# Performance work log

Measured on AMD Instinct MI355X. Metric: run time of the kernel, lower is better.

## Reference

```python
import jax, jax.numpy as jnp
import numpy as np

B, H, W, K, PAD = 1024, 28, 28, 3, 1


def conv3x3(x, w, b):
    out = jax.lax.conv_general_dilated(x, w, (1, 1), ((PAD, PAD), (PAD, PAD)),
                                       dimension_numbers=('NCHW', 'OIHW', 'NCHW'))
    return out + b[None, :, None, None]


def deform_conv2d(x, offset, w, b):
    # torchvision deform_conv2d semantics, stride=1, pad=1, dilation=1, groups=1
    Bn, Cin, Hh, Ww = x.shape
    Cout = w.shape[0]
    KK = K * K
    off = offset.reshape(Bn, KK, 2, Hh, Ww)
    dy, dx = off[:, :, 0], off[:, :, 1]                      # [B,KK,H,W]
    ky, kx = jnp.meshgrid(jnp.arange(K, dtype=x.dtype), jnp.arange(K, dtype=x.dtype), indexing='ij')
    py = dy + (jnp.arange(Hh, dtype=x.dtype) - PAD)[None, None, :, None] + ky.reshape(KK)[None, :, None, None]
    px = dx + (jnp.arange(Ww, dtype=x.dtype) - PAD)[None, None, None, :] + kx.reshape(KK)[None, :, None, None]
    y0 = jnp.floor(py); x0 = jnp.floor(px)
    wy1 = py - y0; wy0 = 1.0 - wy1
    wx1 = px - x0; wx0 = 1.0 - wx1
    xf = x.reshape(Bn, Cin, Hh * Ww)

    def gather(yi, xi):
        valid = (yi >= 0) & (yi < Hh) & (xi >= 0) & (xi < Ww)
        yc = jnp.clip(yi, 0, Hh - 1).astype(jnp.int32)
        xc = jnp.clip(xi, 0, Ww - 1).astype(jnp.int32)
        idx = (yc * Ww + xc).reshape(Bn, -1)                 # [B, KK*H*W]
        g = jnp.take_along_axis(xf, jnp.broadcast_to(idx[:, None, :], (Bn, Cin, idx.shape[1])), axis=2)
        return g.reshape(Bn, Cin, KK, Hh, Ww) * valid.astype(x.dtype)[:, None]

    sampled = (gather(y0, x0) * (wy0 * wx0)[:, None]
               + gather(y0, x0 + 1) * (wy0 * wx1)[:, None]
               + gather(y0 + 1, x0) * (wy1 * wx0)[:, None]
               + gather(y0 + 1, x0 + 1) * (wy1 * wx1)[:, None])  # [B,Cin,KK,H,W]
    out = jnp.einsum('bkhw,ok->bohw', sampled.reshape(Bn, Cin * KK, Hh, Ww),
                     w.reshape(Cout, Cin * KK))
    return out + b[None, :, None, None]


def adaptive_avg_pool_14(x):
    Bn, C, Hh, Ww = x.shape
    f = Hh // 14
    return x.reshape(Bn, C, 14, f, 14, f).mean(axis=(3, 5))


def setup_inputs() -> dict:
    key = jax.random.key(0)
    ks = jax.random.split(key, 14)
    d = {}
    d['x'] = jax.random.normal(ks[0], (B, 1, H, W), dtype=jnp.float32)
    # offset conv 1: Conv2d(1, 18, 3, pad=1)
    d['ow1'] = jax.random.normal(ks[1], (18, 1, 3, 3), dtype=jnp.float32) * 0.1
    d['ob1'] = jnp.zeros((18,), jnp.float32)
    d['w1'] = jax.random.normal(ks[2], (32, 1, 3, 3), dtype=jnp.float32) * 0.01
    d['b1'] = jnp.zeros((32,), jnp.float32)
    # offset conv 2: Conv2d(32, 18, 3, pad=1)
    d['ow2'] = jax.random.normal(ks[3], (18, 32, 3, 3), dtype=jnp.float32) * 0.05
    d['ob2'] = jnp.zeros((18,), jnp.float32)
    d['w2'] = jax.random.normal(ks[4], (64, 32, 3, 3), dtype=jnp.float32) * 0.01
    d['b2'] = jnp.zeros((64,), jnp.float32)
    d['fw1'] = jax.random.normal(ks[5], (128, 64 * 14 * 14), dtype=jnp.float32) * 0.01
    d['fb1'] = jnp.zeros((128,), jnp.float32)
    d['fw2'] = jax.random.normal(ks[6], (10, 128), dtype=jnp.float32) * 0.05
    d['fb2'] = jnp.zeros((10,), jnp.float32)
    return d


def reference(x, ow1, ob1, w1, b1, ow2, ob2, w2, b2, fw1, fb1, fw2, fb2):
    # block1 + relu + pool 28->14
    h = deform_conv2d(x, conv3x3(x, ow1, ob1), w1, b1)
    h = adaptive_avg_pool_14(jax.nn.relu(h))
    # block2 + relu + pool 14->14 (identity)
    h = deform_conv2d(h, conv3x3(h, ow2, ob2), w2, b2)
    h = adaptive_avg_pool_14(jax.nn.relu(h))
    h = h.reshape(h.shape[0], -1)
    # classifier (ExcitationDropout is identity in eval mode)
    h = jax.nn.relu(h @ fw1.T + fb1)
    return h @ fw2.T + fb2
```

## Files before the change

### kernel.cpp

```cpp
#include <hip/hip_runtime.h>

#define NB 1024
#define TOTAL1 (NB*196)

#define WS_H1   0
#define WS_H2   6422528
#define WS_PART 19267584
#define WS_W1T  23461888
#define WS_OW1T 23462176
#define WS_W2T  23462338
#define WS_OW2T 23480770

__global__ __launch_bounds__(256) void prep(const float* __restrict__ w1,
                                            const float* __restrict__ ow1,
                                            const float* __restrict__ w2,
                                            const float* __restrict__ ow2,
                                            float* __restrict__ ws) {
  int i = blockIdx.x * 256 + threadIdx.x;
  if (i < 288)   { int co = i / 9,  kk = i % 9;   ws[WS_W1T  + kk * 32 + co] = w1[i]; }
  if (i < 162)   { int c  = i / 9,  j  = i % 9;   ws[WS_OW1T + j  * 18 + c ] = ow1[i]; }
  if (i < 18432) { int co = i / 288, k = i % 288; ws[WS_W2T  + k  * 64 + co] = w2[i]; }
  if (i < 5184)  { int c  = i / 288, k = i % 288; ws[WS_OW2T + k  * 18 + c ] = ow2[i]; }
}

__global__ __launch_bounds__(256, 2) void stage1(const float* __restrict__ x,
                                                 const float* __restrict__ ob1,
                                                 const float* __restrict__ b1,
                                                 const float* __restrict__ ws,
                                                 float* __restrict__ h1) {
  __shared__ float ximg[3 * 784];
  const float* __restrict__ w1t  = ws + WS_W1T;
  const float* __restrict__ ow1t = ws + WS_OW1T;
  int tid = threadIdx.x;
  int g0 = blockIdx.x * 256;
  int bfirst = g0 / 196;
  for (int idx = tid; idx < 3 * 784; idx += 256) {
    int img = idx / 784;
    int b = bfirst + img;
    ximg[idx] = (b < NB) ? x[b * 784 + (idx - img * 784)] : 0.f;
  }
  __syncthreads();
  int g = g0 + tid;
  if (g >= TOTAL1) return;
  int b = g / 196, p = g - b * 196;
  const float* im = ximg + (b - bfirst) * 784;
  int oy = p / 14, ox = p - (p / 14) * 14;

  float pooled[32];
#pragma unroll
  for (int co = 0; co < 32; ++co) pooled[co] = 0.f;

  for (int sub = 0; sub < 4; ++sub) {
    int y  = 2 * oy + (sub >> 1);
    int ix = 2 * ox + (sub & 1);
    float patch[9];
#pragma unroll
    for (int j = 0; j < 9; ++j) {
      int yy = y + j / 3 - 1, xc = ix + j % 3 - 1;
      bool ok = (yy >= 0) & (yy < 28) & (xc >= 0) & (xc < 28);
      patch[j] = ok ? im[yy * 28 + xc] : 0.f;
    }
    float off[18];
#pragma unroll
    for (int c = 0; c < 18; ++c) off[c] = ob1[c];
#pragma unroll
    for (int j = 0; j < 9; ++j) {
      float v = patch[j];
#pragma unroll
      for (int c = 0; c < 18; ++c) off[c] = fmaf(v, ow1t[j * 18 + c], off[c]);
    }
    float a[32];
#pragma unroll
    for (int co = 0; co < 32; ++co) a[co] = b1[co];
#pragma unroll
    for (int kk = 0; kk < 9; ++kk) {
      float py = (float)(y - 1 + kk / 3) + off[2 * kk];
      float px = (float)(ix - 1 + kk % 3) + off[2 * kk + 1];
      float y0f = floorf(py), x0f = floorf(px);
      float wy1 = py - y0f, wx1 = px - x0f;
      float wy0 = 1.f - wy1, wx0 = 1.f - wx1;
      int y0 = (int)y0f, x0 = (int)x0f;
      int y1 = y0 + 1, x1 = x0 + 1;
      bool vy0 = (y0 >= 0) & (y0 < 28), vy1 = (y1 >= 0) & (y1 < 28);
      bool vx0 = (x0 >= 0) & (x0 < 28), vx1 = (x1 >= 0) & (x1 < 28);
      float W00 = (vy0 & vx0) ? wy0 * wx0 : 0.f;
      float W01 = (vy0 & vx1) ? wy0 * wx1 : 0.f;
      float W10 = (vy1 & vx0) ? wy1 * wx0 : 0.f;
      float W11 = (vy1 & vx1) ? wy1 * wx1 : 0.f;
      int yc0 = min(max(y0, 0), 27), yc1 = min(max(y1, 0), 27);
      int xc0 = min(max(x0, 0), 27), xc1 = min(max(x1, 0), 27);
      float s = im[yc0 * 28 + xc0] * W00 + im[yc0 * 28 + xc1] * W01 +
                im[yc1 * 28 + xc0] * W10 + im[yc1 * 28 + xc1] * W11;
#pragma unroll
      for (int co = 0; co < 32; ++co) a[co] = fmaf(s, w1t[kk * 32 + co], a[co]);
    }
#pragma unroll
    for (int co = 0; co < 32; ++co) pooled[co] += fmaxf(a[co], 0.f);
  }
#pragma unroll
  for (int co = 0; co < 32; ++co) h1[b * 6272 + co * 196 + p] = pooled[co] * 0.25f;
}

__global__ __launch_bounds__(256, 4) void stage2(const float* __restrict__ h1,
                                                 const float* __restrict__ ob2,
                                                 const float* __restrict__ b2,
                                                 const float* __restrict__ ws,
                                                 float* __restrict__ h2) {
  __shared__ float imgT[196 * 32];
  __shared__ float Sbuf2[2 * 1608];
  const float* __restrict__ w2t  = ws + WS_W2T;
  const float* __restrict__ ow2t = ws + WS_OW2T;
  int tid = threadIdx.x;
  int b = blockIdx.x;

  for (int e = tid; e < 6272; e += 256) {
    int ci = e / 196, p = e - ci * 196;
    imgT[p * 32 + ((ci + 4 * p) & 31)] = h1[b * 6272 + e];
  }

  int pp = tid;
  int spy = pp / 14, spx = pp - (pp / 14) * 14;
  bool samp = (pp < 196);

  int cog = tid & 15, pg = tid >> 4;
  int co0 = cog * 4, p0 = pg * 16;
  bool gact = (pg < 13);
  float acc[4][16];
  {
    float4 bb = *(const float4*)(b2 + co0);
    float bj[4] = {bb.x, bb.y, bb.z, bb.w};
#pragma unroll
    for (int jj = 0; jj < 4; ++jj)
#pragma unroll
      for (int i = 0; i < 16; ++i) acc[jj][i] = bj[jj];
  }

  __syncthreads();

  float off[18];
#pragma unroll
  for (int c = 0; c < 18; ++c) off[c] = ob2[c];
  if (samp) {
    for (int j = 0; j < 9; ++j) {
      int yy = spy + j / 3 - 1, xx = spx + j % 3 - 1;
      bool ok = (yy >= 0) & (yy < 14) & (xx >= 0) & (xx < 14);
      int nidx = ok ? (yy * 14 + xx) : 0;
      const float* src = imgT + nidx * 32;
      int rot = (4 * nidx) & 31;
      for (int cq = 0; cq < 8; ++cq) {
        float4 v;
        if (ok) v = *(const float4*)(src + ((cq * 4 + rot) & 31));
        else    v = make_float4(0.f, 0.f, 0.f, 0.f);
        const float* wo0 = ow2t + ((cq * 4 + 0) * 9 + j) * 18;
        const float* wo1 = ow2t + ((cq * 4 + 1) * 9 + j) * 18;
        const float* wo2 = ow2t + ((cq * 4 + 2) * 9 + j) * 18;
        const float* wo3 = ow2t + ((cq * 4 + 3) * 9 + j) * 18;
#pragma unroll
        for (int c = 0; c < 18; ++c) {
          off[c] = fmaf(v.x, wo0[c], off[c]);
          off[c] = fmaf(v.y, wo1[c], off[c]);
          off[c] = fmaf(v.z, wo2[c], off[c]);
          off[c] = fmaf(v.w, wo3[c], off[c]);
        }
      }
    }
  }

  float W00 = 0.f, W01 = 0.f, W10 = 0.f, W11 = 0.f;
  int s00o = 0, s01o = 0, s10o = 0, s11o = 0;
  int r00 = 0, r01 = 0, r10 = 0, r11 = 0;

  auto coeff = [&](int kkv) {
    float dy = off[0], dx = off[1];
#pragma unroll
    for (int t = 1; t < 9; ++t) if (kkv == t) { dy = off[2 * t]; dx = off[2 * t + 1]; }
    float pyv = (float)(spy - 1 + kkv / 3) + dy;
    float pxv = (float)(spx - 1 + kkv % 3) + dx;
    float y0f = floorf(pyv), x0f = floorf(pxv);
    float wy1 = pyv - y0f, wx1 = pxv - x0f;
    float wy0 = 1.f - wy1, wx0 = 1.f - wx1;
    int y0 = (int)y0f, x0 = (int)x0f;
    int y1 = y0 + 1, x1 = x0 + 1;
    bool vy0 = (y0 >= 0) & (y0 < 14), vy1 = (y1 >= 0) & (y1 < 14);
    bool vx0 = (x0 >= 0) & (x0 < 14), vx1 = (x1 >= 0) & (x1 < 14);
    W00 = (vy0 & vx0) ? wy0 * wx0 : 0.f;
    W01 = (vy0 & vx1) ? wy0 * wx1 : 0.f;
    W10 = (vy1 & vx0) ? wy1 * wx0 : 0.f;
    W11 = (vy1 & vx1) ? wy1 * wx1 : 0.f;
    int yc0 = min(max(y0, 0), 13), yc1 = min(max(y1, 0), 13);
    int xc0 = min(max(x0, 0), 13), xc1 = min(max(x1, 0), 13);
    int i00 = yc0 * 14 + xc0, i01 = yc0 * 14 + xc1;
    int i10 = yc1 * 14 + xc0, i11 = yc1 * 14 + xc1;
    s00o = i00 * 32; r00 = (4 * i00) & 31;
    s01o = i01 * 32; r01 = (4 * i01) & 31;
    s10o = i10 * 32; r10 = (4 * i10) & 31;
    s11o = i11 * 32; r11 = (4 * i11) & 31;
  };

  auto sample = [&](int qn, int bufn) {
    float* dst = Sbuf2 + bufn * 1608 + pp;
#pragma unroll
    for (int cg = 0; cg < 2; ++cg) {
      int gq = qn * 2 + cg;
      float4 a0 = *(const float4*)(imgT + s00o + ((gq * 4 + r00) & 31));
      float4 a1 = *(const float4*)(imgT + s01o + ((gq * 4 + r01) & 31));
      float4 a2 = *(const float4*)(imgT + s10o + ((gq * 4 + r10) & 31));
      float4 a3 = *(const float4*)(imgT + s11o + ((gq * 4 + r11) & 31));
      dst[(cg * 4 + 0) * 200] = fmaf(W00, a0.x, fmaf(W01, a1.x, fmaf(W10, a2.x, W11 * a3.x)));
      dst[(cg * 4 + 1) * 200] = fmaf(W00, a0.y, fmaf(W01, a1.y, fmaf(W10, a2.y, W11 * a3.y)));
      dst[(cg * 4 + 2) * 200] = fmaf(W00, a0.z, fmaf(W01, a1.z, fmaf(W10, a2.z, W11 * a3.z)));
      dst[(cg * 4 + 3) * 200] = fmaf(W00, a0.w, fmaf(W01, a1.w, fmaf(W10, a2.w, W11 * a3.w)));
    }
  };

  if (samp) { coeff(0); sample(0, 0); }
  __syncthreads();

  for (int kk = 0; kk < 9; ++kk) {
#pragma unroll
    for (int q = 0; q < 4; ++q) {
      if (samp && !((kk == 8) & (q == 3))) {
        if (q == 3) coeff(kk + 1);
        sample((q + 1) & 3, (q + 1) & 1);
      }
      if (gact) {
        const float* sb = Sbuf2 + (q & 1) * 1608 + p0;
        const float* wb = w2t + kk * 64 + co0;
#pragma unroll 2
        for (int l = 0; l < 8; ++l) {
          int ci = q * 8 + l;
          float4 w = *(const float4*)(wb + ci * 576);
          const float* srow = sb + l * 200;
          float4 s0 = *(const float4*)(srow);
          float4 s1 = *(const float4*)(srow + 4);
          float4 s2 = *(const float4*)(srow + 8);
          float4 s3 = *(const float4*)(srow + 12);
          float sv[16] = {s0.x, s0.y, s0.z, s0.w, s1.x, s1.y, s1.z, s1.w,
                          s2.x, s2.y, s2.z, s2.w, s3.x, s3.y, s3.z, s3.w};
          float wj[4] = {w.x, w.y, w.z, w.w};
#pragma unroll
          for (int jj = 0; jj < 4; ++jj)
#pragma unroll
            for (int i = 0; i < 16; ++i)
              acc[jj][i] = fmaf(wj[jj], sv[i], acc[jj][i]);
        }
      }
      __syncthreads();
    }
  }

  if (gact) {
    float* __restrict__ orow = h2 + b * 12544 + co0 * 196 + p0;
#pragma unroll
    for (int jj = 0; jj < 4; ++jj) {
#pragma unroll
      for (int t = 0; t < 4; ++t) {
        if (p0 + 4 * t < 196) {
          float4 v;
          v.x = fmaxf(acc[jj][4 * t + 0], 0.f);
          v.y = fmaxf(acc[jj][4 * t + 1], 0.f);
          v.z = fmaxf(acc[jj][4 * t + 2], 0.f);
          v.w = fmaxf(acc[jj][4 * t + 3], 0.f);
          *(float4*)(orow + jj * 196 + 4 * t) = v;
        }
      }
    }
  }
}

__global__ __launch_bounds__(256, 2) void fc1(const float* __restrict__ h2,
                                              const float* __restrict__ fw1,
                                              float* __restrict__ part) {
  __shared__ float a_s[56 * 72];
  __shared__ float b_s[56 * 132];
  int tid = threadIdx.x;
  int rb = (blockIdx.x & 15) * 64;
  int ks = blockIdx.x >> 4;
  int kbase = ks * 392;
  int c0 = (tid & 31) * 4;
  int r0 = (tid >> 5) * 8;

  float acc[8][4];
#pragma unroll
  for (int i = 0; i < 8; ++i)
#pragma unroll
    for (int j = 0; j < 4; ++j) acc[i][j] = 0.f;

  for (int ch = 0; ch < 7; ++ch) {
    int kb = kbase + ch * 56;
    __syncthreads();
#pragma unroll
    for (int t = 0; t < 14; ++t) {
      int idx = t * 256 + tid;
      int r = idx / 56, k = idx - r * 56;
      a_s[k * 72 + r] = h2[(rb + r) * 12544 + kb + k];
    }
#pragma unroll
    for (int t = 0; t < 28; ++t) {
      int idx = t * 256 + tid;
      int c = idx / 56, k = idx - c * 56;
      b_s[k * 132 + c] = fw1[c * 12544 + kb + k];
    }
    __syncthreads();
    for (int k = 0; k < 56; ++k) {
      float4 bv = *(const float4*)&b_s[k * 132 + c0];
      float4 av0 = *(const float4*)&a_s[k * 72 + r0];
      float4 av1 = *(const float4*)&a_s[k * 72 + r0 + 4];
      float av[8] = {av0.x, av0.y, av0.z, av0.w, av1.x, av1.y, av1.z, av1.w};
      float bj[4] = {bv.x, bv.y, bv.z, bv.w};
#pragma unroll
      for (int i = 0; i < 8; ++i)
#pragma unroll
        for (int j = 0; j < 4; ++j) acc[i][j] = fmaf(av[i], bj[j], acc[i][j]);
    }
  }
#pragma unroll
  for (int i = 0; i < 8; ++i) {
    int r = rb + r0 + i;
#pragma unroll
    for (int j = 0; j < 4; ++j)
      part[(ks * 1024 + r) * 128 + c0 + j] = acc[i][j];
  }
}

__global__ __launch_bounds__(128) void fcfinal(const float* __restrict__ part,
                                               const float* __restrict__ fb1,
                                               const float* __restrict__ fw2,
                                               const float* __restrict__ fb2,
                                               float* __restrict__ out) {
  __shared__ float tbuf[128];
  int b = blockIdx.x, c = threadIdx.x;
  float s = fb1[c];
  for (int ks = 0; ks < 32; ++ks) s += part[(ks * 1024 + b) * 128 + c];
  tbuf[c] = fmaxf(s, 0.f);
  __syncthreads();
  if (c < 10) {
    float v = fb2[c];
#pragma unroll
    for (int k = 0; k < 128; ++k) v = fmaf(tbuf[k], fw2[c * 128 + k], v);
    out[b * 10 + c] = v;
  }
}

extern "C" void kernel_launch(void* const* d_in, const int* in_sizes, int n_in,
                              void* d_out, int out_size, void* d_ws, size_t ws_size,
                              hipStream_t stream) {
  const float* x   = (const float*)d_in[0];
  const float* ow1 = (const float*)d_in[1];
  const float* ob1 = (const float*)d_in[2];
  const float* w1  = (const float*)d_in[3];
  const float* b1  = (const float*)d_in[4];
  const float* ow2 = (const float*)d_in[5];
  const float* ob2 = (const float*)d_in[6];
  const float* w2  = (const float*)d_in[7];
  const float* b2  = (const float*)d_in[8];
  const float* fw1 = (const float*)d_in[9];
  const float* fb1 = (const float*)d_in[10];
  const float* fw2 = (const float*)d_in[11];
  const float* fb2 = (const float*)d_in[12];
  float* ws  = (float*)d_ws;
  float* out = (float*)d_out;

  prep<<<72, 256, 0, stream>>>(w1, ow1, w2, ow2, ws);
  stage1<<<784, 256, 0, stream>>>(x, ob1, b1, ws, ws + WS_H1);
  stage2<<<NB, 256, 0, stream>>>(ws + WS_H1, ob2, b2, ws, ws + WS_H2);
  fc1<<<512, 256, 0, stream>>>(ws + WS_H2, fw1, ws + WS_PART);
  fcfinal<<<1024, 128, 0, stream>>>(ws + WS_PART, fb1, fw2, fb2, out);
}
```

Before: 443.1 us.

## Split stage2 offset convolution into a separate kernel writing offsets to workspace

Moves the second offset 3x3 conv (32->18 channels) out of stage2 into a new offconv kernel that processes two images per 448-thread block and writes 18 offset maps to the workspace. Stage2 then loads only the dy/dx pair for the next kernel tap from global memory, which frees the 18 offset registers and removes the idle-thread imbalance where only 196 of 256 threads did the offset conv. The cost is an extra kernel launch, a second read of h1, and a global round trip for the offsets. The offsets reuse the WS_PART region, which is safe only because fc1 overwrites it later.

```diff
diff --git a/kernel.cpp b/kernel.cpp
--- a/kernel.cpp
+++ b/kernel.cpp
@@ -6,6 +6,7 @@
 #define WS_H1   0
 #define WS_H2   6422528
 #define WS_PART 19267584
+#define WS_OFF2 WS_PART
 #define WS_W1T  23461888
 #define WS_OW1T 23462176
 #define WS_W2T  23462338
@@ -101,15 +102,72 @@
   for (int co = 0; co < 32; ++co) h1[b * 6272 + co * 196 + p] = pooled[co] * 0.25f;
 }
 
+__global__ __launch_bounds__(448, 4) void offconv(const float* __restrict__ h1,
+                                                  const float* __restrict__ ob2,
+                                                  const float* __restrict__ ws,
+                                                  float* __restrict__ off2) {
+  __shared__ float imgT[2 * 6272];
+  const float* __restrict__ ow2t = ws + WS_OW2T;
+  int tid = threadIdx.x;
+  int bb = blockIdx.x;
+
+  for (int e = tid; e < 12544; e += 448) {
+    int img = e / 6272, rem = e - img * 6272;
+    int ci = rem / 196, p = rem - ci * 196;
+    imgT[img * 6272 + p * 32 + ((ci + 4 * p) & 31)] = h1[bb * 12544 + e];
+  }
+  __syncthreads();
+
+  int img  = tid / 224;
+  int slot = tid - img * 224;
+  int py  = slot >> 4;
+  int pxc = slot & 15;
+  int pxx = min(pxc, 13);
+  int p   = py * 14 + pxx;
+  const float* im = imgT + img * 6272;
+
+  float off[18];
+#pragma unroll
+  for (int c = 0; c < 18; ++c) off[c] = ob2[c];
+  for (int j = 0; j < 9; ++j) {
+    int yy = py + j / 3 - 1, xx = pxx + j % 3 - 1;
+    bool ok = (yy >= 0) & (yy < 14) & (xx >= 0) & (xx < 14);
+    int nidx = ok ? (yy * 14 + xx) : 0;
+    const float* src = im + nidx * 32;
+    int rot = (4 * nidx) & 31;
+    for (int cq = 0; cq < 8; ++cq) {
+      float4 v;
+      if (ok) v = *(const float4*)(src + ((cq * 4 + rot) & 31));
+      else    v = make_float4(0.f, 0.f, 0.f, 0.f);
+      const float* w0 = ow2t + ((cq * 4 + 0) * 9 + j) * 18;
+      const float* w1 = ow2t + ((cq * 4 + 1) * 9 + j) * 18;
+      const float* w2 = ow2t + ((cq * 4 + 2) * 9 + j) * 18;
+      const float* w3 = ow2t + ((cq * 4 + 3) * 9 + j) * 18;
+#pragma unroll
+      for (int c = 0; c < 18; ++c) {
+        off[c] = fmaf(v.x, w0[c], off[c]);
+        off[c] = fmaf(v.y, w1[c], off[c]);
+        off[c] = fmaf(v.z, w2[c], off[c]);
+        off[c] = fmaf(v.w, w3[c], off[c]);
+      }
+    }
+  }
+
+  if (pxc < 14) {
+    float* dst = off2 + (2 * bb + img) * 3528 + p;
+#pragma unroll
+    for (int c = 0; c < 18; ++c) dst[c * 196] = off[c];
+  }
+}
+
 __global__ __launch_bounds__(256, 4) void stage2(const float* __restrict__ h1,
-                                                 const float* __restrict__ ob2,
+                                                 const float* __restrict__ off2,
                                                  const float* __restrict__ b2,
                                                  const float* __restrict__ ws,
                                                  float* __restrict__ h2) {
   __shared__ float imgT[196 * 32];
   __shared__ float Sbuf2[2 * 1608];
-  const float* __restrict__ w2t  = ws + WS_W2T;
-  const float* __restrict__ ow2t = ws + WS_OW2T;
+  const float* __restrict__ w2t = ws + WS_W2T;
   int tid = threadIdx.x;
   int b = blockIdx.x;
 
@@ -121,6 +179,7 @@
   int pp = tid;
   int spy = pp / 14, spx = pp - (pp / 14) * 14;
   bool samp = (pp < 196);
+  const float* off_b = off2 + b * 3528;
 
   int cog = tid & 15, pg = tid >> 4;
   int co0 = cog * 4, p0 = pg * 16;
@@ -135,47 +194,14 @@
       for (int i = 0; i < 16; ++i) acc[jj][i] = bj[jj];
   }
 
-  __syncthreads();
-
-  float off[18];
-#pragma unroll
-  for (int c = 0; c < 18; ++c) off[c] = ob2[c];
-  if (samp) {
-    for (int j = 0; j < 9; ++j) {
-      int yy = spy + j / 3 - 1, xx = spx + j % 3 - 1;
-      bool ok = (yy >= 0) & (yy < 14) & (xx >= 0) & (xx < 14);
-      int nidx = ok ? (yy * 14 + xx) : 0;
-      const float* src = imgT + nidx * 32;
-      int rot = (4 * nidx) & 31;
-      for (int cq = 0; cq < 8; ++cq) {
-        float4 v;
-        if (ok) v = *(const float4*)(src + ((cq * 4 + rot) & 31));
-        else    v = make_float4(0.f, 0.f, 0.f, 0.f);
-        const float* wo0 = ow2t + ((cq * 4 + 0) * 9 + j) * 18;
-        const float* wo1 = ow2t + ((cq * 4 + 1) * 9 + j) * 18;
-        const float* wo2 = ow2t + ((cq * 4 + 2) * 9 + j) * 18;
-        const float* wo3 = ow2t + ((cq * 4 + 3) * 9 + j) * 18;
-#pragma unroll
-        for (int c = 0; c < 18; ++c) {
-          off[c] = fmaf(v.x, wo0[c], off[c]);
-          off[c] = fmaf(v.y, wo1[c], off[c]);
-          off[c] = fmaf(v.z, wo2[c], off[c]);
-          off[c] = fmaf(v.w, wo3[c], off[c]);
-        }
-      }
-    }
-  }
-
   float W00 = 0.f, W01 = 0.f, W10 = 0.f, W11 = 0.f;
   int s00o = 0, s01o = 0, s10o = 0, s11o = 0;
   int r00 = 0, r01 = 0, r10 = 0, r11 = 0;
+  float dyn = 0.f, dxn = 0.f;
 
   auto coeff = [&](int kkv) {
-    float dy = off[0], dx = off[1];
-#pragma unroll
-    for (int t = 1; t < 9; ++t) if (kkv == t) { dy = off[2 * t]; dx = off[2 * t + 1]; }
-    float pyv = (float)(spy - 1 + kkv / 3) + dy;
-    float pxv = (float)(spx - 1 + kkv % 3) + dx;
+    float pyv = (float)(spy - 1 + kkv / 3) + dyn;
+    float pxv = (float)(spx - 1 + kkv % 3) + dxn;
     float y0f = floorf(pyv), x0f = floorf(pxv);
     float wy1 = pyv - y0f, wx1 = pxv - x0f;
     float wy0 = 1.f - wy1, wx0 = 1.f - wx1;
@@ -213,6 +239,8 @@
     }
   };
 
+  if (samp) { dyn = off_b[pp]; dxn = off_b[196 + pp]; }
+  __syncthreads();
   if (samp) { coeff(0); sample(0, 0); }
   __syncthreads();
 
@@ -220,6 +248,10 @@
 #pragma unroll
     for (int q = 0; q < 4; ++q) {
       if (samp && !((kk == 8) & (q == 3))) {
+        if (q == 1 && kk < 8) {
+          dyn = off_b[(2 * kk + 2) * 196 + pp];
+          dxn = off_b[(2 * kk + 3) * 196 + pp];
+        }
         if (q == 3) coeff(kk + 1);
         sample((q + 1) & 3, (q + 1) & 1);
       }
@@ -363,7 +395,8 @@
 
   prep<<<72, 256, 0, stream>>>(w1, ow1, w2, ow2, ws);
   stage1<<<784, 256, 0, stream>>>(x, ob1, b1, ws, ws + WS_H1);
-  stage2<<<NB, 256, 0, stream>>>(ws + WS_H1, ob2, b2, ws, ws + WS_H2);
+  offconv<<<512, 448, 0, stream>>>(ws + WS_H1, ob2, ws, ws + WS_OFF2);
+  stage2<<<NB, 256, 0, stream>>>(ws + WS_H1, ws + WS_OFF2, b2, ws, ws + WS_H2);
   fc1<<<512, 256, 0, stream>>>(ws + WS_H2, fw1, ws + WS_PART);
   fcfinal<<<1024, 128, 0, stream>>>(ws + WS_PART, fb1, fw2, fb2, out);
 }
```

Result: no change. 448.4 us (+1.2%).

## Compute stage2 offset conv as a cooperative shared-memory GEMM and retile main GEMM to 8x8

Applied to the files above, without the earlier changes.

The offset convolution in stage2 no longer has each sampling thread accumulate all 18 offset channels serially from global weights. Instead, all threads run it as a tiled GEMM over double-buffered im2col patches staged in shared memory, with each thread owning one offset channel and 16 pixels. Per-tap dy/dx offsets are written into a small shared buffer just before the main loop needs them, which frees the 18 live offset registers. The main deformable GEMM tile changes from 4x16 to 8x8 per thread to rebalance shared-memory reads against FMAs. The cost is an extra phase with 36 barriers and more shared-memory traffic.

```diff
diff --git a/kernel.cpp b/kernel.cpp
--- a/kernel.cpp
+++ b/kernel.cpp
@@ -108,6 +108,7 @@
                                                  float* __restrict__ h2) {
   __shared__ float imgT[196 * 32];
   __shared__ float Sbuf2[2 * 1608];
+  __shared__ float offT[2 * 208];
   const float* __restrict__ w2t  = ws + WS_W2T;
   const float* __restrict__ ow2t = ws + WS_OW2T;
   int tid = threadIdx.x;
@@ -122,48 +123,87 @@
   int spy = pp / 14, spx = pp - (pp / 14) * 14;
   bool samp = (pp < 196);
 
-  int cog = tid & 15, pg = tid >> 4;
-  int co0 = cog * 4, p0 = pg * 16;
-  bool gact = (pg < 13);
-  float acc[4][16];
+  int oc  = tid % 18;
+  int opg = tid / 18;
+  int op0 = opg * 16;
+  bool oact = (tid < 234);
+  float myob = oact ? ob2[oc] : 0.f;
+  float oacc[16];
+#pragma unroll
+  for (int i = 0; i < 16; ++i) oacc[i] = 0.f;
+
+  int cog = tid & 7, pg = tid >> 3;
+  int co0 = cog * 8, p0 = pg * 8;
+  bool gact = (pg < 25);
+
+  auto p2sample = [&](int j, int qn, int bufn) {
+    int yy = spy + j / 3 - 1, xx = spx + j % 3 - 1;
+    bool ok = (yy >= 0) & (yy < 14) & (xx >= 0) & (xx < 14);
+    int nidx = ok ? (yy * 14 + xx) : 0;
+    const float* src = imgT + nidx * 32;
+    int rot = (4 * nidx) & 31;
+    float* dst = Sbuf2 + bufn * 1608 + pp;
+#pragma unroll
+    for (int cg = 0; cg < 2; ++cg) {
+      int gq = qn * 2 + cg;
+      float4 v;
+      if (ok) v = *(const float4*)(src + ((gq * 4 + rot) & 31));
+      else    v = make_float4(0.f, 0.f, 0.f, 0.f);
+      dst[(cg * 4 + 0) * 200] = v.x;
+      dst[(cg * 4 + 1) * 200] = v.y;
+      dst[(cg * 4 + 2) * 200] = v.z;
+      dst[(cg * 4 + 3) * 200] = v.w;
+    }
+  };
+
+  __syncthreads();
+
+  if (samp) p2sample(0, 0, 0);
+  __syncthreads();
+  for (int j = 0; j < 9; ++j) {
+#pragma unroll
+    for (int q = 0; q < 4; ++q) {
+      if (samp && !((j == 8) & (q == 3))) {
+        int nj = (q == 3) ? j + 1 : j;
+        p2sample(nj, (q + 1) & 3, (q + 1) & 1);
+      }
+      if (oact) {
+        const float* sb = Sbuf2 + (q & 1) * 1608 + op0;
+#pragma unroll 2
+        for (int l = 0; l < 8; ++l) {
+          int ci = q * 8 + l;
+          float w = ow2t[(ci * 9 + j) * 18 + oc];
+          const float* srow = sb + l * 200;
+#pragma unroll
+          for (int t = 0; t < 4; ++t) {
+            float4 s = *(const float4*)(srow + 4 * t);
+            oacc[4 * t + 0] = fmaf(w, s.x, oacc[4 * t + 0]);
+            oacc[4 * t + 1] = fmaf(w, s.y, oacc[4 * t + 1]);
+            oacc[4 * t + 2] = fmaf(w, s.z, oacc[4 * t + 2]);
+            oacc[4 * t + 3] = fmaf(w, s.w, oacc[4 * t + 3]);
+          }
+        }
+      }
+      __syncthreads();
+    }
+  }
+
+  if (oact && (oc >> 1) == 0) {
+    float* dst = offT + (oc & 1) * 208 + op0;
+#pragma unroll
+    for (int i = 0; i < 16; ++i) dst[i] = oacc[i] + myob;
+  }
+  __syncthreads();
+
+  float acc[8][8];
   {
-    float4 bb = *(const float4*)(b2 + co0);
-    float bj[4] = {bb.x, bb.y, bb.z, bb.w};
-#pragma unroll
-    for (int jj = 0; jj < 4; ++jj)
-#pragma unroll
-      for (int i = 0; i < 16; ++i) acc[jj][i] = bj[jj];
-  }
-
-  __syncthreads();
-
-  float off[18];
-#pragma unroll
-  for (int c = 0; c < 18; ++c) off[c] = ob2[c];
-  if (samp) {
-    for (int j = 0; j < 9; ++j) {
-      int yy = spy + j / 3 - 1, xx = spx + j % 3 - 1;
-      bool ok = (yy >= 0) & (yy < 14) & (xx >= 0) & (xx < 14);
-      int nidx = ok ? (yy * 14 + xx) : 0;
-      const float* src = imgT + nidx * 32;
-      int rot = (4 * nidx) & 31;
-      for (int cq = 0; cq < 8; ++cq) {
-        float4 v;
-        if (ok) v = *(const float4*)(src + ((cq * 4 + rot) & 31));
-        else    v = make_float4(0.f, 0.f, 0.f, 0.f);
-        const float* wo0 = ow2t + ((cq * 4 + 0) * 9 + j) * 18;
-        const float* wo1 = ow2t + ((cq * 4 + 1) * 9 + j) * 18;
-        const float* wo2 = ow2t + ((cq * 4 + 2) * 9 + j) * 18;
-        const float* wo3 = ow2t + ((cq * 4 + 3) * 9 + j) * 18;
-#pragma unroll
-        for (int c = 0; c < 18; ++c) {
-          off[c] = fmaf(v.x, wo0[c], off[c]);
-          off[c] = fmaf(v.y, wo1[c], off[c]);
-          off[c] = fmaf(v.z, wo2[c], off[c]);
-          off[c] = fmaf(v.w, wo3[c], off[c]);
-        }
-      }
-    }
+    float4 ba = *(const float4*)(b2 + co0);
+    float4 bbv = *(const float4*)(b2 + co0 + 4);
+    float bj[8] = {ba.x, ba.y, ba.z, ba.w, bbv.x, bbv.y, bbv.z, bbv.w};
+#pragma unroll
+    for (int jj = 0; jj < 8; ++jj)
+#pragma unroll
+      for (int i = 0; i < 8; ++i) acc[jj][i] = bj[jj];
   }
 
   float W00 = 0.f, W01 = 0.f, W10 = 0.f, W11 = 0.f;
@@ -171,11 +211,10 @@
   int r00 = 0, r01 = 0, r10 = 0, r11 = 0;
 
   auto coeff = [&](int kkv) {
-    float dy = off[0], dx = off[1];
-#pragma unroll
-    for (int t = 1; t < 9; ++t) if (kkv == t) { dy = off[2 * t]; dx = off[2 * t + 1]; }
-    float pyv = (float)(spy - 1 + kkv / 3) + dy;
-    float pxv = (float)(spx - 1 + kkv % 3) + dx;
+    float dyv = offT[pp];
+    float dxv = offT[208 + pp];
+    float pyv = (float)(spy - 1 + kkv / 3) + dyv;
+    float pxv = (float)(spx - 1 + kkv % 3) + dxv;
     float y0f = floorf(pyv), x0f = floorf(pxv);
     float wy1 = pyv - y0f, wx1 = pxv - x0f;
     float wy0 = 1.f - wy1, wx0 = 1.f - wx1;
@@ -229,22 +268,25 @@
 #pragma unroll 2
         for (int l = 0; l < 8; ++l) {
           int ci = q * 8 + l;
-          float4 w = *(const float4*)(wb + ci * 576);
+          float4 wa = *(const float4*)(wb + ci * 576);
+          float4 wbv = *(const float4*)(wb + ci * 576 + 4);
           const float* srow = sb + l * 200;
           float4 s0 = *(const float4*)(srow);
           float4 s1 = *(const float4*)(srow + 4);
-          float4 s2 = *(const float4*)(srow + 8);
-          float4 s3 = *(const float4*)(srow + 12);
-          float sv[16] = {s0.x, s0.y, s0.z, s0.w, s1.x, s1.y, s1.z, s1.w,
-                          s2.x, s2.y, s2.z, s2.w, s3.x, s3.y, s3.z, s3.w};
-          float wj[4] = {w.x, w.y, w.z, w.w};
-#pragma unroll
-          for (int jj = 0; jj < 4; ++jj)
-#pragma unroll
-            for (int i = 0; i < 16; ++i)
+          float sv[8] = {s0.x, s0.y, s0.z, s0.w, s1.x, s1.y, s1.z, s1.w};
+          float wj[8] = {wa.x, wa.y, wa.z, wa.w, wbv.x, wbv.y, wbv.z, wbv.w};
+#pragma unroll
+          for (int jj = 0; jj < 8; ++jj)
+#pragma unroll
+            for (int i = 0; i < 8; ++i)
               acc[jj][i] = fmaf(wj[jj], sv[i], acc[jj][i]);
         }
       }
+      if (q == 2 && kk < 8 && oact && (oc >> 1) == (kk + 1)) {
+        float* dst = offT + (oc & 1) * 208 + op0;
+#pragma unroll
+        for (int i = 0; i < 16; ++i) dst[i] = oacc[i] + myob;
+      }
       __syncthreads();
     }
   }
@@ -252,17 +294,20 @@
   if (gact) {
     float* __restrict__ orow = h2 + b * 12544 + co0 * 196 + p0;
 #pragma unroll
-    for (int jj = 0; jj < 4; ++jj) {
-#pragma unroll
-      for (int t = 0; t < 4; ++t) {
-        if (p0 + 4 * t < 196) {
-          float4 v;
-          v.x = fmaxf(acc[jj][4 * t + 0], 0.f);
-          v.y = fmaxf(acc[jj][4 * t + 1], 0.f);
-          v.z = fmaxf(acc[jj][4 * t + 2], 0.f);
-          v.w = fmaxf(acc[jj][4 * t + 3], 0.f);
-          *(float4*)(orow + jj * 196 + 4 * t) = v;
-        }
+    for (int jj = 0; jj < 8; ++jj) {
+      float4 v0;
+      v0.x = fmaxf(acc[jj][0], 0.f);
+      v0.y = fmaxf(acc[jj][1], 0.f);
+      v0.z = fmaxf(acc[jj][2], 0.f);
+      v0.w = fmaxf(acc[jj][3], 0.f);
+      *(float4*)(orow + jj * 196) = v0;
+      if (p0 + 4 < 196) {
+        float4 v1;
+        v1.x = fmaxf(acc[jj][4], 0.f);
+        v1.y = fmaxf(acc[jj][5], 0.f);
+        v1.z = fmaxf(acc[jj][6], 0.f);
+        v1.w = fmaxf(acc[jj][7], 0.f);
+        *(float4*)(orow + jj * 196 + 4) = v1;
       }
     }
   }
```

After: 403.9 us. 8.8% less time.
